# Kernel tuning notes

Hardware: AMD Instinct MI355X
Metric: run time of the kernel (lower is better)

The kernel has to match this reference:

```python
import jax, jax.numpy as jnp
import numpy as np

H = 128  # hidden_size
I = 28   # input_size
C = 10   # num_classes


def setup_inputs() -> dict:
    key = jax.random.key(0)
    ks = jax.random.split(key, 11)
    s = 1.0 / np.sqrt(H)  # torch nn.RNN init scale
    return {
        "x": jax.random.normal(ks[0], (8192, 28, I), dtype=jnp.float32),
        "W_ih0": jax.random.uniform(ks[1], (H, I), jnp.float32, -s, s),
        "W_hh0": jax.random.uniform(ks[2], (H, H), jnp.float32, -s, s),
        "b_ih0": jax.random.uniform(ks[3], (H,), jnp.float32, -s, s),
        "b_hh0": jax.random.uniform(ks[4], (H,), jnp.float32, -s, s),
        "W_ih1": jax.random.uniform(ks[5], (H, H), jnp.float32, -s, s),
        "W_hh1": jax.random.uniform(ks[6], (H, H), jnp.float32, -s, s),
        "b_ih1": jax.random.uniform(ks[7], (H,), jnp.float32, -s, s),
        "b_hh1": jax.random.uniform(ks[8], (H,), jnp.float32, -s, s),
        "fc_w": jax.random.uniform(ks[9], (C, H), jnp.float32, -s, s),
        "fc_b": jax.random.uniform(ks[10], (C,), jnp.float32, -s, s),
    }


def _rnn_layer_full(x, W_ih, b_ih, W_hh, b_hh):
    # x: [B, T, D] -> full output sequence [B, T, H]
    B = x.shape[0]
    h0 = jnp.zeros((B, H), x.dtype)
    xw = jnp.einsum('btd,hd->bth', x, W_ih) + b_ih  # precompute input GEMM

    def step(h, xw_t):
        h = jnp.tanh(xw_t + h @ W_hh.T + b_hh)
        return h, h

    _, ys = jax.lax.scan(step, h0, jnp.swapaxes(xw, 0, 1))  # [T, B, H]
    return jnp.swapaxes(ys, 0, 1)


def _rnn_layer_last(x, W_ih, b_ih, W_hh, b_hh):
    # only the final hidden state is needed downstream
    B = x.shape[0]
    h0 = jnp.zeros((B, H), x.dtype)
    xw = jnp.einsum('btd,hd->bth', x, W_ih) + b_ih

    def step(h, xw_t):
        h = jnp.tanh(xw_t + h @ W_hh.T + b_hh)
        return h, None

    h_last, _ = jax.lax.scan(step, h0, jnp.swapaxes(xw, 0, 1))
    return h_last


def reference(x, W_ih0, W_hh0, b_ih0, b_hh0, W_ih1, W_hh1, b_ih1, b_hh1, fc_w, fc_b):
    out0 = _rnn_layer_full(x, W_ih0, b_ih0, W_hh0, b_hh0)   # [B, T, H]
    h_last = _rnn_layer_last(out0, W_ih1, b_ih1, W_hh1, b_hh1)  # [B, H] == out[:, -1, :]
    return h_last @ fc_w.T + fc_b  # [B, C]
```

## Files before the change

kernel.cpp:

```cpp
#include <hip/hip_runtime.h>

#define HSZ 128
#define ISZ 28
#define TSZ 28
#define CSZ 10
#define BT  32
#define NG  2
#define NT  512

typedef _Float16 half_t;
typedef _Float16 v8h __attribute__((ext_vector_type(8)));
typedef _Float16 v4h __attribute__((ext_vector_type(4)));
typedef float v4f __attribute__((ext_vector_type(4)));

__device__ __forceinline__ float fast_tanh(float x) {
    float e = __expf(2.f * x);
    return 1.f - 2.f * __builtin_amdgcn_rcpf(e + 1.f);
}

__device__ __forceinline__ int imin(int a, int b) { return a < b ? a : b; }

__global__ __launch_bounds__(NT, 2)
void rnn_pc(const float* __restrict__ x,
            const float* __restrict__ W_ih0, const float* __restrict__ W_hh0,
            const float* __restrict__ b_ih0, const float* __restrict__ b_hh0,
            const float* __restrict__ W_ih1, const float* __restrict__ W_hh1,
            const float* __restrict__ b_ih1, const float* __restrict__ b_hh1,
            const float* __restrict__ fc_w, const float* __restrict__ fc_b,
            float* __restrict__ out)
{
    __shared__ half_t h0r[4][NG][2048];
    __shared__ half_t h1r[4][NG][2048];
    __shared__ half_t xs[TSZ][NG][512];
    __shared__ int    flags[8];

    const int tid  = threadIdx.x;
    const int wave = tid >> 6;
    const int lane = tid & 63;
    const int ln   = lane & 15;
    const int quad = lane >> 4;
    const int b0   = blockIdx.x * BT;
    const int w4   = wave & 3;
    const int wsl  = w4 * 512 + (quad >> 1) * 128 + ln * 8 + (quad & 1) * 4;
    const int ro   = lane * 8;
    volatile int* vf = (volatile int*)flags;

    {
#pragma unroll
        for (int it = 0; it < 7; ++it) {
            const int c = tid + it * NT;
            const int q = c & 3;
            const int n = (c >> 2) & 15;
            const int g = (c >> 6) & 1;
            const int t = c >> 7;
            const float* gp = x + ((size_t)(b0 + g * 16 + n) * TSZ + t) * ISZ + q * 8;
            float4 a = *(const float4*)gp;
            float4 b = (q < 3) ? *(const float4*)(gp + 4) : make_float4(0.f, 0.f, 0.f, 0.f);
            v8h p = {(half_t)a.x, (half_t)a.y, (half_t)a.z, (half_t)a.w,
                     (half_t)b.x, (half_t)b.y, (half_t)b.z, (half_t)b.w};
            *(v8h*)&xs[t][g][(q * 16 + n) * 8] = p;
        }
    }
    {
        const v8h z = {(half_t)0.f, (half_t)0.f, (half_t)0.f, (half_t)0.f,
                       (half_t)0.f, (half_t)0.f, (half_t)0.f, (half_t)0.f};
        *(v8h*)&h0r[3][0][tid * 8] = z;
        *(v8h*)&h1r[3][0][tid * 8] = z;
        if (tid < 8) flags[tid] = 0;
    }
    __syncthreads();

    if (wave < 4) {
        v8h aWx[2], aW0[2][4];
        v4f bias0[2];
#pragma unroll
        for (int rt = 0; rt < 2; ++rt) {
            const int row = w4 * 32 + rt * 16 + ln;
            float4 p = *(const float4*)(b_ih0 + w4 * 32 + rt * 16 + quad * 4);
            float4 q = *(const float4*)(b_hh0 + w4 * 32 + rt * 16 + quad * 4);
            bias0[rt] = (v4f){p.x + q.x, p.y + q.y, p.z + q.z, p.w + q.w};
            const float* pw = W_ih0 + row * ISZ + quad * 8;
            float4 a = *(const float4*)pw;
            float4 b = (quad < 3) ? *(const float4*)(pw + 4) : make_float4(0.f, 0.f, 0.f, 0.f);
            aWx[rt] = (v8h){(half_t)a.x, (half_t)a.y, (half_t)a.z, (half_t)a.w,
                            (half_t)b.x, (half_t)b.y, (half_t)b.z, (half_t)b.w};
#pragma unroll
            for (int ks = 0; ks < 4; ++ks) {
                const float4* p0 = (const float4*)(W_hh0 + row * HSZ + ks * 32 + quad * 8);
                float4 c = p0[0], d = p0[1];
                aW0[rt][ks] = (v8h){(half_t)c.x, (half_t)c.y, (half_t)c.z, (half_t)c.w,
                                    (half_t)d.x, (half_t)d.y, (half_t)d.z, (half_t)d.w};
            }
        }

        for (int t = 0; t < TSZ; ++t) {
            for (;;) {
                int m0 = imin(imin(vf[0], vf[1]), imin(vf[2], vf[3]));
                int m1 = imin(imin(vf[4], vf[5]), imin(vf[6], vf[7]));
                if (m0 >= t && m1 >= t - 3) break;
            }
            __asm__ volatile("" ::: "memory");
            const int sr = (t + 3) & 3, sw = t & 3;
#pragma unroll
            for (int g = 0; g < NG; ++g) {
                v8h bh[4];
#pragma unroll
                for (int ks = 0; ks < 4; ++ks)
                    bh[ks] = *(const v8h*)&h0r[sr][g][ks * 512 + ro];
                const v8h bx = *(const v8h*)&xs[t][g][ro];
#pragma unroll
                for (int rt = 0; rt < 2; ++rt) {
                    v4f c = bias0[rt];
                    c = __builtin_amdgcn_mfma_f32_16x16x32_f16(aWx[rt], bx, c, 0, 0, 0);
#pragma unroll
                    for (int ks = 0; ks < 4; ++ks)
                        c = __builtin_amdgcn_mfma_f32_16x16x32_f16(aW0[rt][ks], bh[ks], c, 0, 0, 0);
                    v4h p = {(half_t)fast_tanh(c[0]), (half_t)fast_tanh(c[1]),
                             (half_t)fast_tanh(c[2]), (half_t)fast_tanh(c[3])};
                    *(v4h*)&h0r[sw][g][wsl + rt * 256] = p;
                }
            }
            __asm__ volatile("s_waitcnt lgkmcnt(0)" ::: "memory");
            if (lane == 0) vf[w4] = t + 1;
        }
    } else {
        v8h aW1i[2][4], aW1h[2][4];
        v4f bias1[2];
#pragma unroll
        for (int rt = 0; rt < 2; ++rt) {
            const int row = w4 * 32 + rt * 16 + ln;
            float4 p = *(const float4*)(b_ih1 + w4 * 32 + rt * 16 + quad * 4);
            float4 q = *(const float4*)(b_hh1 + w4 * 32 + rt * 16 + quad * 4);
            bias1[rt] = (v4f){p.x + q.x, p.y + q.y, p.z + q.z, p.w + q.w};
#pragma unroll
            for (int ks = 0; ks < 4; ++ks) {
                const float4* p1 = (const float4*)(W_ih1 + row * HSZ + ks * 32 + quad * 8);
                const float4* p2 = (const float4*)(W_hh1 + row * HSZ + ks * 32 + quad * 8);
                float4 a = p1[0], b = p1[1];
                aW1i[rt][ks] = (v8h){(half_t)a.x, (half_t)a.y, (half_t)a.z, (half_t)a.w,
                                     (half_t)b.x, (half_t)b.y, (half_t)b.z, (half_t)b.w};
                a = p2[0]; b = p2[1];
                aW1h[rt][ks] = (v8h){(half_t)a.x, (half_t)a.y, (half_t)a.z, (half_t)a.w,
                                     (half_t)b.x, (half_t)b.y, (half_t)b.z, (half_t)b.w};
            }
        }

        for (int t = 0; t < TSZ; ++t) {
            for (;;) {
                int m0 = imin(imin(vf[0], vf[1]), imin(vf[2], vf[3]));
                int m1 = imin(imin(vf[4], vf[5]), imin(vf[6], vf[7]));
                if (m0 >= t + 1 && m1 >= t) break;
            }
            __asm__ volatile("" ::: "memory");
            const int s0 = t & 3, s1 = (t + 3) & 3;
#pragma unroll
            for (int g = 0; g < NG; ++g) {
                v8h bh0[4], bh1[4];
#pragma unroll
                for (int ks = 0; ks < 4; ++ks) {
                    bh0[ks] = *(const v8h*)&h0r[s0][g][ks * 512 + ro];
                    bh1[ks] = *(const v8h*)&h1r[s1][g][ks * 512 + ro];
                }
#pragma unroll
                for (int rt = 0; rt < 2; ++rt) {
                    v4f si = bias1[rt];
                    v4f sh = (v4f){0.f, 0.f, 0.f, 0.f};
#pragma unroll
                    for (int ks = 0; ks < 4; ++ks) {
                        si = __builtin_amdgcn_mfma_f32_16x16x32_f16(aW1i[rt][ks], bh0[ks], si, 0, 0, 0);
                        sh = __builtin_amdgcn_mfma_f32_16x16x32_f16(aW1h[rt][ks], bh1[ks], sh, 0, 0, 0);
                    }
                    const v4f a1 = si + sh;
                    v4h p = {(half_t)fast_tanh(a1[0]), (half_t)fast_tanh(a1[1]),
                             (half_t)fast_tanh(a1[2]), (half_t)fast_tanh(a1[3])};
                    *(v4h*)&h1r[s0][g][wsl + rt * 256] = p;
                }
            }
            __asm__ volatile("s_waitcnt lgkmcnt(0)" ::: "memory");
            if (lane == 0) vf[4 + w4] = t + 1;
        }
    }
    __syncthreads();

    if (tid < BT * CSZ) {
        const int m = tid / CSZ, cc = tid - m * CSZ;
        const int g = m >> 4, n = m & 15;
        float s = fc_b[cc];
#pragma unroll
        for (int ks = 0; ks < 4; ++ks) {
#pragma unroll
            for (int q2 = 0; q2 < 4; ++q2) {
                const v8h hv = *(const v8h*)&h1r[3][g][(ks * 64 + q2 * 16 + n) * 8];
                const int kb = ks * 32 + q2 * 8;
                const float4 w0 = *(const float4*)(fc_w + cc * HSZ + kb);
                const float4 w1 = *(const float4*)(fc_w + cc * HSZ + kb + 4);
                s += (float)hv[0] * w0.x + (float)hv[1] * w0.y +
                     (float)hv[2] * w0.z + (float)hv[3] * w0.w +
                     (float)hv[4] * w1.x + (float)hv[5] * w1.y +
                     (float)hv[6] * w1.z + (float)hv[7] * w1.w;
            }
        }
        out[(b0 + m) * CSZ + cc] = s;
    }
}

extern "C" void kernel_launch(void* const* d_in, const int* in_sizes, int n_in,
                              void* d_out, int out_size, void* d_ws, size_t ws_size,
                              hipStream_t stream) {
    const float* x     = (const float*)d_in[0];
    const float* W_ih0 = (const float*)d_in[1];
    const float* W_hh0 = (const float*)d_in[2];
    const float* b_ih0 = (const float*)d_in[3];
    const float* b_hh0 = (const float*)d_in[4];
    const float* W_ih1 = (const float*)d_in[5];
    const float* W_hh1 = (const float*)d_in[6];
    const float* b_ih1 = (const float*)d_in[7];
    const float* b_hh1 = (const float*)d_in[8];
    const float* fc_w  = (const float*)d_in[9];
    const float* fc_b  = (const float*)d_in[10];
    float* out = (float*)d_out;

    const int B = in_sizes[0] / (TSZ * ISZ);
    dim3 grid(B / BT), block(NT);
    rnn_pc<<<grid, block, 0, stream>>>(x, W_ih0, W_hh0, b_ih0, b_hh0,
                                       W_ih1, W_hh1, b_ih1, b_hh1,
                                       fc_w, fc_b, out);
}
```

Measured before the change: 131.6 us.

## Repartition RNN waves by batch group with per-group flag sync and folded bias

Reorganizes the block from 8 waves to 6. Each layer-0 wave now owns one batch group and computes all 128 hidden rows, so it only waits on its own layer-1 consumers. Layer-1 work is split across four waves, one per group and output half, and each synchronizes only with its partner wave and its layer-0 producer. The layer-0 bias is folded into the padded input column, a constant 1 in x times the bias in W_ih0, which removes the separate bias add. Layer-0 waves get raised priority and spin-waits now sleep; the tradeoff is higher register pressure and a longer serial MFMA chain per layer-0 wave.

```diff
diff --git a/kernel.cpp b/kernel.cpp
--- a/kernel.cpp
+++ b/kernel.cpp
@@ -6,7 +6,7 @@
 #define CSZ 10
 #define BT  32
 #define NG  2
-#define NT  512
+#define NT  384
 
 typedef _Float16 half_t;
 typedef _Float16 v8h __attribute__((ext_vector_type(8)));
@@ -17,11 +17,10 @@
     float e = __expf(2.f * x);
     return 1.f - 2.f * __builtin_amdgcn_rcpf(e + 1.f);
 }
-
 __device__ __forceinline__ int imin(int a, int b) { return a < b ? a : b; }
 
 __global__ __launch_bounds__(NT, 2)
-void rnn_pc(const float* __restrict__ x,
+void rnn_ws(const float* __restrict__ x,
             const float* __restrict__ W_ih0, const float* __restrict__ W_hh0,
             const float* __restrict__ b_ih0, const float* __restrict__ b_hh0,
             const float* __restrict__ W_ih1, const float* __restrict__ W_hh1,
@@ -29,9 +28,9 @@
             const float* __restrict__ fc_w, const float* __restrict__ fc_b,
             float* __restrict__ out)
 {
+    __shared__ half_t xs[TSZ][NG][512];
     __shared__ half_t h0r[4][NG][2048];
     __shared__ half_t h1r[4][NG][2048];
-    __shared__ half_t xs[TSZ][NG][512];
     __shared__ int    flags[8];
 
     const int tid  = threadIdx.x;
@@ -40,22 +39,20 @@
     const int ln   = lane & 15;
     const int quad = lane >> 4;
     const int b0   = blockIdx.x * BT;
-    const int w4   = wave & 3;
-    const int wsl  = w4 * 512 + (quad >> 1) * 128 + ln * 8 + (quad & 1) * 4;
     const int ro   = lane * 8;
+    const int wbq  = (quad >> 1) * 128 + ln * 8 + (quad & 1) * 4;
     volatile int* vf = (volatile int*)flags;
 
-    {
-#pragma unroll
-        for (int it = 0; it < 7; ++it) {
-            const int c = tid + it * NT;
+    for (int it = 0; it < 10; ++it) {
+        const int c = tid + it * NT;
+        if (c < TSZ * 128) {
             const int q = c & 3;
             const int n = (c >> 2) & 15;
             const int g = (c >> 6) & 1;
             const int t = c >> 7;
             const float* gp = x + ((size_t)(b0 + g * 16 + n) * TSZ + t) * ISZ + q * 8;
             float4 a = *(const float4*)gp;
-            float4 b = (q < 3) ? *(const float4*)(gp + 4) : make_float4(0.f, 0.f, 0.f, 0.f);
+            float4 b = (q < 3) ? *(const float4*)(gp + 4) : make_float4(1.f, 0.f, 0.f, 0.f);
             v8h p = {(half_t)a.x, (half_t)a.y, (half_t)a.z, (half_t)a.w,
                      (half_t)b.x, (half_t)b.y, (half_t)b.z, (half_t)b.w};
             *(v8h*)&xs[t][g][(q * 16 + n) * 8] = p;
@@ -64,24 +61,25 @@
     {
         const v8h z = {(half_t)0.f, (half_t)0.f, (half_t)0.f, (half_t)0.f,
                        (half_t)0.f, (half_t)0.f, (half_t)0.f, (half_t)0.f};
-        *(v8h*)&h0r[3][0][tid * 8] = z;
-        *(v8h*)&h1r[3][0][tid * 8] = z;
+        for (int idx = tid; idx < 512; idx += NT) {
+            *(v8h*)&h0r[3][0][idx * 8] = z;
+            *(v8h*)&h1r[3][0][idx * 8] = z;
+        }
         if (tid < 8) flags[tid] = 0;
     }
     __syncthreads();
 
-    if (wave < 4) {
-        v8h aWx[2], aW0[2][4];
-        v4f bias0[2];
-#pragma unroll
-        for (int rt = 0; rt < 2; ++rt) {
-            const int row = w4 * 32 + rt * 16 + ln;
-            float4 p = *(const float4*)(b_ih0 + w4 * 32 + rt * 16 + quad * 4);
-            float4 q = *(const float4*)(b_hh0 + w4 * 32 + rt * 16 + quad * 4);
-            bias0[rt] = (v4f){p.x + q.x, p.y + q.y, p.z + q.z, p.w + q.w};
+    if (wave < NG) {
+        const int g = wave;
+        v8h aWx[8], aW0[8][4];
+#pragma unroll
+        for (int rt = 0; rt < 8; ++rt) {
+            const int row = rt * 16 + ln;
+            const float bias = b_ih0[row] + b_hh0[row];
             const float* pw = W_ih0 + row * ISZ + quad * 8;
             float4 a = *(const float4*)pw;
-            float4 b = (quad < 3) ? *(const float4*)(pw + 4) : make_float4(0.f, 0.f, 0.f, 0.f);
+            float4 b = (quad < 3) ? *(const float4*)(pw + 4)
+                                  : make_float4(bias, 0.f, 0.f, 0.f);
             aWx[rt] = (v8h){(half_t)a.x, (half_t)a.y, (half_t)a.z, (half_t)a.w,
                             (half_t)b.x, (half_t)b.y, (half_t)b.z, (half_t)b.w};
 #pragma unroll
@@ -92,45 +90,54 @@
                                     (half_t)d.x, (half_t)d.y, (half_t)d.z, (half_t)d.w};
             }
         }
+        __builtin_amdgcn_s_setprio(1);
 
         for (int t = 0; t < TSZ; ++t) {
-            for (;;) {
-                int m0 = imin(imin(vf[0], vf[1]), imin(vf[2], vf[3]));
-                int m1 = imin(imin(vf[4], vf[5]), imin(vf[6], vf[7]));
-                if (m0 >= t && m1 >= t - 3) break;
+            if (t >= 4) {
+                while (imin(vf[2 + 2 * g], vf[3 + 2 * g]) < t - 3)
+                    __builtin_amdgcn_s_sleep(1);
             }
             __asm__ volatile("" ::: "memory");
             const int sr = (t + 3) & 3, sw = t & 3;
-#pragma unroll
-            for (int g = 0; g < NG; ++g) {
-                v8h bh[4];
-#pragma unroll
-                for (int ks = 0; ks < 4; ++ks)
-                    bh[ks] = *(const v8h*)&h0r[sr][g][ks * 512 + ro];
-                const v8h bx = *(const v8h*)&xs[t][g][ro];
-#pragma unroll
-                for (int rt = 0; rt < 2; ++rt) {
-                    v4f c = bias0[rt];
-                    c = __builtin_amdgcn_mfma_f32_16x16x32_f16(aWx[rt], bx, c, 0, 0, 0);
-#pragma unroll
-                    for (int ks = 0; ks < 4; ++ks)
-                        c = __builtin_amdgcn_mfma_f32_16x16x32_f16(aW0[rt][ks], bh[ks], c, 0, 0, 0);
-                    v4h p = {(half_t)fast_tanh(c[0]), (half_t)fast_tanh(c[1]),
-                             (half_t)fast_tanh(c[2]), (half_t)fast_tanh(c[3])};
-                    *(v4h*)&h0r[sw][g][wsl + rt * 256] = p;
-                }
+
+            v8h bh[4];
+#pragma unroll
+            for (int ks = 0; ks < 4; ++ks)
+                bh[ks] = *(const v8h*)&h0r[sr][g][ks * 512 + ro];
+            const v8h bx = *(const v8h*)&xs[t][g][ro];
+
+            v4f acc[8];
+#pragma unroll
+            for (int rt = 0; rt < 8; ++rt)
+                acc[rt] = __builtin_amdgcn_mfma_f32_16x16x32_f16(
+                    aWx[rt], bx, (v4f){0.f, 0.f, 0.f, 0.f}, 0, 0, 0);
+#pragma unroll
+            for (int ks = 0; ks < 4; ++ks)
+#pragma unroll
+                for (int rt = 0; rt < 8; ++rt)
+                    acc[rt] = __builtin_amdgcn_mfma_f32_16x16x32_f16(
+                        aW0[rt][ks], bh[ks], acc[rt], 0, 0, 0);
+#pragma unroll
+            for (int rt = 0; rt < 8; ++rt) {
+                v4h p = {(half_t)fast_tanh(acc[rt][0]), (half_t)fast_tanh(acc[rt][1]),
+                         (half_t)fast_tanh(acc[rt][2]), (half_t)fast_tanh(acc[rt][3])};
+                *(v4h*)&h0r[sw][g][(rt >> 1) * 512 + (rt & 1) * 256 + wbq] = p;
             }
             __asm__ volatile("s_waitcnt lgkmcnt(0)" ::: "memory");
-            if (lane == 0) vf[w4] = t + 1;
-        }
+            if (lane == 0) vf[g] = t + 1;
+        }
+        __builtin_amdgcn_s_setprio(0);
     } else {
-        v8h aW1i[2][4], aW1h[2][4];
-        v4f bias1[2];
-#pragma unroll
-        for (int rt = 0; rt < 2; ++rt) {
-            const int row = w4 * 32 + rt * 16 + ln;
-            float4 p = *(const float4*)(b_ih1 + w4 * 32 + rt * 16 + quad * 4);
-            float4 q = *(const float4*)(b_hh1 + w4 * 32 + rt * 16 + quad * 4);
+        const int q4 = wave - 2;
+        const int g  = q4 >> 1;
+        const int c  = q4 & 1;
+        v8h aW1i[4][4], aW1h[4][4];
+        v4f bias1[4];
+#pragma unroll
+        for (int rt = 0; rt < 4; ++rt) {
+            const int row = c * 64 + rt * 16 + ln;
+            float4 p = *(const float4*)(b_ih1 + c * 64 + rt * 16 + quad * 4);
+            float4 q = *(const float4*)(b_hh1 + c * 64 + rt * 16 + quad * 4);
             bias1[rt] = (v4f){p.x + q.x, p.y + q.y, p.z + q.z, p.w + q.w};
 #pragma unroll
             for (int ks = 0; ks < 4; ++ks) {
@@ -146,38 +153,43 @@
         }
 
         for (int t = 0; t < TSZ; ++t) {
-            for (;;) {
-                int m0 = imin(imin(vf[0], vf[1]), imin(vf[2], vf[3]));
-                int m1 = imin(imin(vf[4], vf[5]), imin(vf[6], vf[7]));
-                if (m0 >= t + 1 && m1 >= t) break;
-            }
+            const int pid = 2 + 2 * g + (c ^ 1);
+            while (vf[g] < t + 1 || vf[pid] < t)
+                __builtin_amdgcn_s_sleep(1);
             __asm__ volatile("" ::: "memory");
             const int s0 = t & 3, s1 = (t + 3) & 3;
-#pragma unroll
-            for (int g = 0; g < NG; ++g) {
-                v8h bh0[4], bh1[4];
-#pragma unroll
-                for (int ks = 0; ks < 4; ++ks) {
-                    bh0[ks] = *(const v8h*)&h0r[s0][g][ks * 512 + ro];
-                    bh1[ks] = *(const v8h*)&h1r[s1][g][ks * 512 + ro];
+
+            v8h bh0[4], bh1[4];
+#pragma unroll
+            for (int ks = 0; ks < 4; ++ks) {
+                bh0[ks] = *(const v8h*)&h0r[s0][g][ks * 512 + ro];
+                bh1[ks] = *(const v8h*)&h1r[s1][g][ks * 512 + ro];
+            }
+            v4f si[4], sh[4];
+#pragma unroll
+            for (int rt = 0; rt < 4; ++rt) {
+                si[rt] = bias1[rt];
+                sh[rt] = (v4f){0.f, 0.f, 0.f, 0.f};
+            }
+#pragma unroll
+            for (int ks = 0; ks < 4; ++ks)
+#pragma unroll
+                for (int rt = 0; rt < 4; ++rt) {
+                    si[rt] = __builtin_amdgcn_mfma_f32_16x16x32_f16(
+                        aW1i[rt][ks], bh0[ks], si[rt], 0, 0, 0);
+                    sh[rt] = __builtin_amdgcn_mfma_f32_16x16x32_f16(
+                        aW1h[rt][ks], bh1[ks], sh[rt], 0, 0, 0);
                 }
 #pragma unroll
-                for (int rt = 0; rt < 2; ++rt) {
-                    v4f si = bias1[rt];
-                    v4f sh = (v4f){0.f, 0.f, 0.f, 0.f};
-#pragma unroll
-                    for (int ks = 0; ks < 4; ++ks) {
-                        si = __builtin_amdgcn_mfma_f32_16x16x32_f16(aW1i[rt][ks], bh0[ks], si, 0, 0, 0);
-                        sh = __builtin_amdgcn_mfma_f32_16x16x32_f16(aW1h[rt][ks], bh1[ks], sh, 0, 0, 0);
-                    }
-                    const v4f a1 = si + sh;
-                    v4h p = {(half_t)fast_tanh(a1[0]), (half_t)fast_tanh(a1[1]),
-                             (half_t)fast_tanh(a1[2]), (half_t)fast_tanh(a1[3])};
-                    *(v4h*)&h1r[s0][g][wsl + rt * 256] = p;
-                }
+            for (int rt = 0; rt < 4; ++rt) {
+                const v4f a1 = si[rt] + sh[rt];
+                const int rtg = c * 4 + rt;
+                v4h p = {(half_t)fast_tanh(a1[0]), (half_t)fast_tanh(a1[1]),
+                         (half_t)fast_tanh(a1[2]), (half_t)fast_tanh(a1[3])};
+                *(v4h*)&h1r[s0][g][(rtg >> 1) * 512 + (rtg & 1) * 256 + wbq] = p;
             }
             __asm__ volatile("s_waitcnt lgkmcnt(0)" ::: "memory");
-            if (lane == 0) vf[4 + w4] = t + 1;
+            if (lane == 0) vf[2 + 2 * g + c] = t + 1;
         }
     }
     __syncthreads();
@@ -222,7 +234,7 @@
 
     const int B = in_sizes[0] / (TSZ * ISZ);
     dim3 grid(B / BT), block(NT);
-    rnn_pc<<<grid, block, 0, stream>>>(x, W_ih0, W_hh0, b_ih0, b_hh0,
+    rnn_ws<<<grid, block, 0, stream>>>(x, W_ih0, W_hh0, b_ih0, b_hh0,
                                        W_ih1, W_hh1, b_ih1, b_hh1,
                                        fc_w, fc_b, out);
 }
```

Measured after the change: 152.8 us. +16.2%, slower.
